# Kernel optimization log

Measured on AMD Instinct MI355X. Metric: run time of the kernel, lower is better.

The kernel has to match this reference:

```python
import jax, jax.numpy as jnp
import numpy as np

HEADS = 8
MEM_LEN = 32


def _mha(q, k, v, Wq, bq, Wk, bk, Wv, bv, Wo, bo):
    # torch nn.MultiheadAttention, batch_first=False. q: [Lq,B,E], k/v: [Lk,B,E]
    Lq, B, E = q.shape
    d = E // HEADS

    def proj(t, W, b):
        p = t @ W.T + b
        return p.reshape(t.shape[0], B, HEADS, d).transpose(1, 2, 0, 3)  # [B,h,L,d]

    qh, kh, vh = proj(q, Wq, bq), proj(k, Wk, bk), proj(v, Wv, bv)
    scale = 1.0 / jnp.sqrt(jnp.asarray(d, q.dtype))
    att = jax.nn.softmax(jnp.einsum('bhqd,bhkd->bhqk', qh * scale, kh), axis=-1)
    out = jnp.einsum('bhqk,bhkd->bhqd', att, vh)          # [B,h,Lq,d]
    out = out.transpose(2, 0, 1, 3).reshape(Lq, B, E)
    return out @ Wo.T + bo


def _forward(x, h, c, memK, memV, externalK, externalV,
             W_ih, W_hh, b_ih, b_hh,
             sWq, sbq, sWk, sbk, sWv, sbv, sWo, sbo,
             cWq, cbq, cWk, cbk, cWv, cbv, cWo, cbo,
             Wres, bres, Wrout, brout, Wcomp, bcomp, Wexp, bexp, Wgate, bgate):
    H = h.shape[1]
    # LSTMCell (torch gate order i, f, g, o)
    gates = x @ W_ih.T + b_ih + h @ W_hh.T + b_hh
    i, f, g, o = jnp.split(gates, 4, axis=1)
    c_next = jax.nn.sigmoid(f) * c + jax.nn.sigmoid(i) * jnp.tanh(g)
    h_lstm = jax.nn.sigmoid(o) * jnp.tanh(c_next)
    # append detached h_lstm to short memory, keep last MEM_LEN entries
    cur = jax.lax.stop_gradient(h_lstm)[None]                      # [1,B,H]
    memK_new = jnp.concatenate([memK, cur], axis=0)[-MEM_LEN:]     # [ML,B,H]
    memV_new = jnp.concatenate([memV, cur], axis=0)[-MEM_LEN:]
    qSelf = h_lstm[None]                                           # [1,B,H]
    self_out = _mha(qSelf, memK_new, memV_new, sWq, sbq, sWk, sbk, sWv, sbv, sWo, sbo)[0]
    ext_out = _mha(qSelf, externalK, externalV, cWq, cbq, cWk, cbk, cWv, cbv, cWo, cbo)[0]
    rw = jax.nn.softmax(h_lstm @ Wrout.T + brout, axis=1)          # [B,2] router
    routed_attn = rw[:, :1] * self_out + rw[:, 1:2] * ext_out
    routed = h_lstm + routed_attn + routed_attn @ Wres.T + bres
    temporal_summary = memK_new.mean(axis=0)                       # [B,H]
    compressed = temporal_summary @ Wcomp.T + bcomp                # [B,H//4]
    expanded = compressed @ Wexp.T + bexp                          # [B,H]
    reps = -(-H // compressed.shape[1])
    compressed_expanded = jnp.tile(compressed, (1, reps))[:, :H]
    gate = jax.nn.sigmoid(jnp.concatenate([x, routed], axis=1) @ Wgate.T + bgate)
    hCT = compressed_expanded + gate * (expanded - compressed_expanded)  # torch.lerp
    hFinal = (h_lstm + routed + hCT) / 3.0                         # dropout = identity (eval)
    return hFinal, h_lstm, c_next


def setup_inputs() -> dict:
    key = jax.random.key(0)
    ks = jax.random.split(key, 34)
    B, I, H, ML, EL = 2048, 1024, 1024, 32, 32
    BN = H // 4
    rn = lambda k, s, sc=1.0: jax.random.normal(k, s, dtype=jnp.float32) * sc
    return {
        'x': rn(ks[0], (B, I)), 'h': rn(ks[1], (B, H)), 'c': rn(ks[2], (B, H)),
        'memK': rn(ks[3], (ML, B, H)), 'memV': rn(ks[4], (ML, B, H)),
        'externalK': rn(ks[5], (EL, B, H)), 'externalV': rn(ks[6], (EL, B, H)),
        'W_ih': rn(ks[7], (4 * H, I), 0.02), 'W_hh': rn(ks[8], (4 * H, H), 0.02),
        'b_ih': jnp.zeros((4 * H,), jnp.float32), 'b_hh': jnp.zeros((4 * H,), jnp.float32),
        'sWq': rn(ks[9], (H, H), 0.02), 'sbq': rn(ks[10], (H,), 0.02),
        'sWk': rn(ks[11], (H, H), 0.02), 'sbk': rn(ks[12], (H,), 0.02),
        'sWv': rn(ks[13], (H, H), 0.02), 'sbv': rn(ks[14], (H,), 0.02),
        'sWo': rn(ks[15], (H, H), 0.02), 'sbo': rn(ks[16], (H,), 0.02),
        'cWq': rn(ks[17], (H, H), 0.02), 'cbq': rn(ks[18], (H,), 0.02),
        'cWk': rn(ks[19], (H, H), 0.02), 'cbk': rn(ks[20], (H,), 0.02),
        'cWv': rn(ks[21], (H, H), 0.02), 'cbv': rn(ks[22], (H,), 0.02),
        'cWo': rn(ks[23], (H, H), 0.02), 'cbo': rn(ks[24], (H,), 0.02),
        'Wres': rn(ks[25], (H, H), 0.02), 'bres': rn(ks[26], (H,), 0.02),
        'Wrout': rn(ks[27], (2, H), 0.02), 'brout': rn(ks[28], (2,), 0.02),
        'Wcomp': rn(ks[29], (BN, H), 0.02), 'bcomp': rn(ks[30], (BN,), 0.02),
        'Wexp': rn(ks[31], (H, BN), 0.02), 'bexp': rn(ks[32], (H,), 0.02),
        'Wgate': rn(ks[33], (H, I + H), 0.02), 'bgate': jnp.zeros((H,), jnp.float32),
    }


def reference(x, h, c, memK, memV, externalK, externalV,
              W_ih, W_hh, b_ih, b_hh,
              sWq, sbq, sWk, sbk, sWv, sbv, sWo, sbo,
              cWq, cbq, cWk, cbk, cWv, cbv, cWo, cbo,
              Wres, bres, Wrout, brout, Wcomp, bcomp, Wexp, bexp, Wgate, bgate):
    return _forward(x, h, c, memK, memV, externalK, externalV,
                    W_ih, W_hh, b_ih, b_hh,
                    sWq, sbq, sWk, sbk, sWv, sbv, sWo, sbo,
                    cWq, cbq, cWk, cbk, cWv, cbv, cWo, cbo,
                    Wres, bres, Wrout, brout, Wcomp, bcomp, Wexp, bexp, Wgate, bgate)
```

## Files before the change

### kernel.cpp

```cpp
#include <hip/hip_runtime.h>
#include <math.h>

typedef __attribute__((ext_vector_type(4))) float f32x4;
typedef __attribute__((ext_vector_type(8))) short bf16x8;
typedef __attribute__((ext_vector_type(4))) unsigned short u16x4;
typedef __attribute__((ext_vector_type(8))) unsigned short u16x8;

__device__ __forceinline__ unsigned short f2bf(float f) {
  unsigned u = __builtin_bit_cast(unsigned, f);
  u += 0x7fffu + ((u >> 16) & 1u);
  return (unsigned short)(u >> 16);
}
__device__ __forceinline__ float bf2f(unsigned short s) {
  return __builtin_bit_cast(float, (unsigned)s << 16);
}
__device__ __forceinline__ float sigmoidf_(float x) { return 1.f / (1.f + __expf(-x)); }

template <int TN, int ACAT, int BCAT, int EPI, int ABF16, int OBF16>
__global__ __launch_bounds__(256) void gemm_k(
    const void* __restrict__ A1, const void* __restrict__ A1b, int lda1, long aZ,
    const void* __restrict__ A2, int lda2, int Ksplit,
    const float* __restrict__ B1, const float* __restrict__ B1b, int ldb1, long bZ,
    const float* __restrict__ B2, int ldb2,
    const float* __restrict__ bias1, const float* __restrict__ bias1b, long biasZ,
    const float* __restrict__ bias2,
    void* __restrict__ C, void* __restrict__ Cb, int ldc, long cZ,
    int K, int zs, float scale,
    const float* __restrict__ P0, const float* __restrict__ P1,
    const float* __restrict__ P2, const float* __restrict__ P3) {
  constexpr int NBI = TN / 32;
  __shared__ unsigned short As[2][128][32];
  __shared__ unsigned short Bs[2][TN][32];
  const int t = threadIdx.x;
  const int lane = t & 63;
  const int wave = t >> 6;
  const int wr = wave >> 1, wc = wave & 1;

  const unsigned gx = gridDim.x, gy = gridDim.y;
  unsigned L = blockIdx.x + gx * (blockIdx.y + gy * blockIdx.z);
  const unsigned nwg = gx * gy * gridDim.z;
  L = (L & 7u) * (nwg >> 3) + (L >> 3);
  const int bn = L % gx;
  const unsigned r1 = L / gx;
  const int bm = r1 % gy;
  const int z = r1 / gy;

  const bool hi = z >= zs;
  const int zz = hi ? z - zs : z;
  const char* Abase = (const char*)(hi ? A1b : A1) + (long)zz * aZ * (ABF16 ? 2 : 4);
  const float* Bbase = (hi ? B1b : B1) + (long)zz * bZ;
  const float* biasp = hi ? bias1b : bias1;
  char* Czc = (char*)(hi ? Cb : C) + (long)zz * cZ * (OBF16 ? 2 : 4);

  const int ar = t >> 3;
  const int bc = (t & 7) * 4;

  const int kIters = K >> 5;
  u16x4 Ra[4], Rb[NBI];

  auto loadT = [&](int kt) {
    const int k0 = kt << 5;
    const char* Ap; int ldA, kA;
    if (ACAT == 1 && k0 >= Ksplit) { Ap = (const char*)A2; ldA = lda2; kA = k0 - Ksplit; }
    else { Ap = Abase; ldA = lda1; kA = k0; }
    const float* Bp; int ldB, kB;
    if (BCAT == 1 && k0 >= Ksplit) { Bp = B2; ldB = ldb2; kB = k0 - Ksplit; }
    else { Bp = Bbase; ldB = ldb1; kB = k0; }
#pragma unroll
    for (int i = 0; i < 4; ++i) {
      const long aoff = ((long)bm * 128 + ar + 32 * i) * ldA + kA + bc;
      if (ABF16) {
        Ra[i] = *(const u16x4*)((const unsigned short*)Ap + aoff);
      } else {
        f32x4 v = *(const f32x4*)((const float*)Ap + aoff);
        u16x4 pk;
        pk[0] = f2bf(v[0]); pk[1] = f2bf(v[1]); pk[2] = f2bf(v[2]); pk[3] = f2bf(v[3]);
        Ra[i] = pk;
      }
    }
#pragma unroll
    for (int i = 0; i < NBI; ++i) {
      f32x4 bv = *(const f32x4*)(Bp + ((long)bn * TN + ar + 32 * i) * ldB + kB + bc);
      u16x4 bp;
      bp[0] = f2bf(bv[0]); bp[1] = f2bf(bv[1]); bp[2] = f2bf(bv[2]); bp[3] = f2bf(bv[3]);
      Rb[i] = bp;
    }
  };

  loadT(0);

  f32x4 acc[4][NBI] = {};
  int p = 0;
  for (int kt = 0; kt < kIters; ++kt) {
    __syncthreads();
#pragma unroll
    for (int i = 0; i < 4; ++i) *(u16x4*)&As[p][ar + 32 * i][bc] = Ra[i];
#pragma unroll
    for (int i = 0; i < NBI; ++i) *(u16x4*)&Bs[p][ar + 32 * i][bc] = Rb[i];
    if (kt + 1 < kIters) loadT(kt + 1);
    __syncthreads();

    bf16x8 af[4], bfr[NBI];
#pragma unroll
    for (int mi = 0; mi < 4; ++mi)
      af[mi] = *(const bf16x8*)&As[p][wr * 64 + mi * 16 + (lane & 15)][(lane >> 4) * 8];
#pragma unroll
    for (int ni = 0; ni < NBI; ++ni)
      bfr[ni] = *(const bf16x8*)&Bs[p][wc * (TN / 2) + ni * 16 + (lane & 15)][(lane >> 4) * 8];
#pragma unroll
    for (int mi = 0; mi < 4; ++mi)
#pragma unroll
      for (int ni = 0; ni < NBI; ++ni)
        acc[mi][ni] = __builtin_amdgcn_mfma_f32_16x16x32_bf16(af[mi], bfr[ni], acc[mi][ni], 0, 0, 0);
    p ^= 1;
  }

  const int colb = bn * TN + wc * (TN / 2);
  const int rowb = bm * 128 + wr * 64;
#pragma unroll
  for (int mi = 0; mi < 4; ++mi) {
#pragma unroll
    for (int ni = 0; ni < NBI; ++ni) {
      f32x4 v = acc[mi][ni];
      const int col = colb + ni * 16 + (lane & 15);
      const int row0 = rowb + mi * 16 + ((lane >> 4) << 2);
      float bsum = 0.f;
      if (biasp) bsum += biasp[zz * biasZ + col];
      if (bias2) bsum += bias2[col];
#pragma unroll
      for (int q = 0; q < 4; ++q) {
        const long row = row0 + q;
        const long off = row * ldc + col;
        const float val = v[q] + bsum;
        if (EPI == 0) {
          if (OBF16) ((unsigned short*)Czc)[off] = f2bf(val * scale);
          else       ((float*)Czc)[off] = val * scale;
        } else if (EPI == 1) {
          ((float*)Czc)[off] = val + P0[off] + P1[off];
        } else if (EPI == 2) {
          const float g = sigmoidf_(val);
          const float ce = P0[row * 256 + (col & 255)];
          const float ex = P1[off];
          ((float*)Czc)[off] = (P2[off] + P3[off] + ce + g * (ex - ce)) * (1.f / 3.f);
        } else if (EPI == 3) {
          ((unsigned short*)Czc)[off] = f2bf(val * P0[2 * row + (hi ? 1 : 0)]);
        } else {
          ((float*)Czc)[off] = val + P2[2 * row] * P0[col] + P2[2 * row + 1] * P1[col];
        }
      }
    }
  }
}

__global__ __launch_bounds__(256) void transpose_k(const float* __restrict__ in0,
                                                   float* __restrict__ out0,
                                                   const float* __restrict__ in1,
                                                   float* __restrict__ out1, int n) {
  __shared__ float tile[64][65];
  const float* in = blockIdx.z ? in1 : in0;
  float* out = blockIdx.z ? out1 : out0;
  const int tr = blockIdx.y, tc = blockIdx.x, t = threadIdx.x;
#pragma unroll
  for (int it = 0; it < 16; ++it) {
    int idx = t + 256 * it;
    int r = idx >> 6, c = idx & 63;
    tile[r][c] = in[(long)(tr * 64 + r) * n + tc * 64 + c];
  }
  __syncthreads();
#pragma unroll
  for (int it = 0; it < 16; ++it) {
    int idx = t + 256 * it;
    int rr = idx >> 6, cc = idx & 63;
    out[(long)(tc * 64 + rr) * n + tr * 64 + cc] = tile[cc][rr];
  }
}

__global__ __launch_bounds__(256) void lstm_k(const float* __restrict__ gates,
                                              const float* __restrict__ c_in,
                                              const float* __restrict__ Wr,
                                              const float* __restrict__ br,
                                              float* __restrict__ c_out,
                                              float* __restrict__ h_ws,
                                              float* __restrict__ h_out,
                                              float* __restrict__ rw) {
  const int b = blockIdx.x, t = threadIdx.x;
  const long base = (long)b * 1024 + t * 4;
  const float* gb = gates + (long)b * 4096 + t * 4;
  f32x4 gi = *(const f32x4*)(gb);
  f32x4 gf = *(const f32x4*)(gb + 1024);
  f32x4 gg = *(const f32x4*)(gb + 2048);
  f32x4 go = *(const f32x4*)(gb + 3072);
  f32x4 cv = *(const f32x4*)(c_in + base);
  f32x4 cn, hv;
#pragma unroll
  for (int q = 0; q < 4; ++q) {
    float cc = sigmoidf_(gf[q]) * cv[q] + sigmoidf_(gi[q]) * tanhf(gg[q]);
    cn[q] = cc;
    hv[q] = sigmoidf_(go[q]) * tanhf(cc);
  }
  *(f32x4*)(c_out + base) = cn;
  *(f32x4*)(h_ws + base) = hv;
  *(f32x4*)(h_out + base) = hv;
  f32x4 w0 = *(const f32x4*)(Wr + t * 4);
  f32x4 w1 = *(const f32x4*)(Wr + 1024 + t * 4);
  float a0 = hv[0] * w0[0] + hv[1] * w0[1] + hv[2] * w0[2] + hv[3] * w0[3];
  float a1 = hv[0] * w1[0] + hv[1] * w1[1] + hv[2] * w1[2] + hv[3] * w1[3];
#pragma unroll
  for (int m = 32; m >= 1; m >>= 1) {
    a0 += __shfl_xor(a0, m);
    a1 += __shfl_xor(a1, m);
  }
  __shared__ float red[8];
  if ((t & 63) == 0) { red[t >> 6] = a0; red[4 + (t >> 6)] = a1; }
  __syncthreads();
  if (t == 0) {
    float z0 = red[0] + red[1] + red[2] + red[3] + br[0];
    float z1 = red[4] + red[5] + red[6] + red[7] + br[1];
    float mx = fmaxf(z0, z1);
    float e0 = __expf(z0 - mx), e1 = __expf(z1 - mx);
    float s = e0 + e1;
    rw[2 * b] = e0 / s;
    rw[2 * b + 1] = e1 / s;
  }
}

__global__ __launch_bounds__(256) void attn5_k(
    const float* __restrict__ memK, const float* __restrict__ memV,
    const float* __restrict__ extK, const float* __restrict__ extV,
    const float* __restrict__ hl,
    const unsigned short* __restrict__ qtS, const unsigned short* __restrict__ qtE,
    unsigned short* __restrict__ mixS, unsigned short* __restrict__ mixE,
    float* __restrict__ ts) {
  const int NB = 2048, H = 1024;
  __shared__ float qtf[8][1028];
  __shared__ float S_lds[32][8];
  __shared__ float P_lds[32][8];
  const int b = blockIdx.x;
  const bool self = blockIdx.y == 0;
  const int t = threadIdx.x;

  auto krow = [&](int r_) -> const float* {
    return self ? ((r_ < 31) ? memK + ((long)(r_ + 1) * NB + b) * H : hl + (long)b * H)
                : extK + ((long)r_ * NB + b) * H;
  };
  auto vrow = [&](int r_) -> const float* {
    return self ? ((r_ < 31) ? memV + ((long)(r_ + 1) * NB + b) * H : hl + (long)b * H)
                : extV + ((long)r_ * NB + b) * H;
  };

  {
    const unsigned short* qtb = (self ? qtS : qtE) + (long)b * 8192;
#pragma unroll
    for (int i = 0; i < 4; ++i) {
      const int idx = t + 256 * i;
      u16x8 qv = *(const u16x8*)(qtb + idx * 8);
      const int hh = idx >> 7, pos = (idx & 127) * 8;
      f32x4 lo, hi2;
      lo[0] = bf2f(qv[0]); lo[1] = bf2f(qv[1]); lo[2] = bf2f(qv[2]); lo[3] = bf2f(qv[3]);
      hi2[0] = bf2f(qv[4]); hi2[1] = bf2f(qv[5]); hi2[2] = bf2f(qv[6]); hi2[3] = bf2f(qv[7]);
      *(f32x4*)&qtf[hh][pos] = lo;
      *(f32x4*)&qtf[hh][pos + 4] = hi2;
    }
  }
  __syncthreads();

  const int r = t >> 3, sub = t & 7;
  const float* Kr = krow(r) + sub * 4;
  float s[8] = {};
#pragma unroll
  for (int j = 0; j < 32; j += 4) {
    f32x4 kc[4];
#pragma unroll
    for (int u = 0; u < 4; ++u) kc[u] = *(const f32x4*)(Kr + (j + u) * 32);
#pragma unroll
    for (int u = 0; u < 4; ++u) {
      const int kk = ((j + u) * 8 + sub) * 4;
#pragma unroll
      for (int hh = 0; hh < 8; ++hh) {
        f32x4 q = *(const f32x4*)&qtf[hh][kk];
        s[hh] += kc[u][0] * q[0] + kc[u][1] * q[1] + kc[u][2] * q[2] + kc[u][3] * q[3];
      }
    }
  }
#pragma unroll
  for (int hh = 0; hh < 8; ++hh) {
    s[hh] += __shfl_xor(s[hh], 1);
    s[hh] += __shfl_xor(s[hh], 2);
    s[hh] += __shfl_xor(s[hh], 4);
  }
  if (sub == 0) {
#pragma unroll
    for (int hh = 0; hh < 8; ++hh) S_lds[r][hh] = s[hh];
  }
  __syncthreads();

  {
    const int rr = t & 31, hh = t >> 5;
    float Sv = S_lds[rr][hh];
    float mx = Sv;
#pragma unroll
    for (int m = 16; m >= 1; m >>= 1) mx = fmaxf(mx, __shfl_xor(mx, m, 32));
    float pr = __expf(Sv - mx);
    float su = pr;
#pragma unroll
    for (int m = 16; m >= 1; m >>= 1) su += __shfl_xor(su, m, 32);
    P_lds[rr][hh] = pr / su;
  }
  __syncthreads();

  if (self) {
    f32x4 a = {};
#pragma unroll
    for (int l = 0; l < 32; ++l) {
      f32x4 kv = *(const f32x4*)(krow(l) + 4 * t);
      a += kv;
    }
    *(f32x4*)(ts + (long)b * H + 4 * t) = a * (1.f / 32.f);
  }

  f32x4 acc[8] = {};
#pragma unroll
  for (int l = 0; l < 32; l += 4) {
    f32x4 vv[4];
#pragma unroll
    for (int u = 0; u < 4; ++u) vv[u] = *(const f32x4*)(vrow(l + u) + 4 * t);
#pragma unroll
    for (int u = 0; u < 4; ++u) {
      f32x4 pa = *(const f32x4*)&P_lds[l + u][0];
      f32x4 pb = *(const f32x4*)&P_lds[l + u][4];
#pragma unroll
      for (int hh = 0; hh < 4; ++hh) {
        acc[hh] += pa[hh] * vv[u];
        acc[4 + hh] += pb[hh] * vv[u];
      }
    }
  }
  unsigned short* mixp = (self ? mixS : mixE) + (long)b * 8192;
#pragma unroll
  for (int hh = 0; hh < 8; ++hh) {
    u16x4 pk;
    pk[0] = f2bf(acc[hh][0]); pk[1] = f2bf(acc[hh][1]);
    pk[2] = f2bf(acc[hh][2]); pk[3] = f2bf(acc[hh][3]);
    *(u16x4*)(mixp + hh * 1024 + 4 * t) = pk;
  }
}

extern "C" void kernel_launch(void* const* d_in, const int* in_sizes, int n_in,
                              void* d_out, int out_size, void* d_ws, size_t ws_size,
                              hipStream_t stream) {
  const float* x    = (const float*)d_in[0];
  const float* h    = (const float*)d_in[1];
  const float* c    = (const float*)d_in[2];
  const float* memK = (const float*)d_in[3];
  const float* memV = (const float*)d_in[4];
  const float* extK = (const float*)d_in[5];
  const float* extV = (const float*)d_in[6];
  const float* W_ih = (const float*)d_in[7];
  const float* W_hh = (const float*)d_in[8];
  const float* b_ih = (const float*)d_in[9];
  const float* b_hh = (const float*)d_in[10];
  const float* sWq = (const float*)d_in[11];
  const float* sbq = (const float*)d_in[12];
  const float* sWk = (const float*)d_in[13];
  const float* sWv = (const float*)d_in[15];
  const float* sbv = (const float*)d_in[16];
  const float* sWo = (const float*)d_in[17];
  const float* sbo = (const float*)d_in[18];
  const float* cWq = (const float*)d_in[19];
  const float* cbq = (const float*)d_in[20];
  const float* cWk = (const float*)d_in[21];
  const float* cWv = (const float*)d_in[23];
  const float* cbv = (const float*)d_in[24];
  const float* cWo = (const float*)d_in[25];
  const float* cbo = (const float*)d_in[26];
  const float* Wres = (const float*)d_in[27];
  const float* bres = (const float*)d_in[28];
  const float* Wrout = (const float*)d_in[29];
  const float* brout = (const float*)d_in[30];
  const float* Wcomp = (const float*)d_in[31];
  const float* bcomp = (const float*)d_in[32];
  const float* Wexp = (const float*)d_in[33];
  const float* bexp = (const float*)d_in[34];
  const float* Wgate = (const float*)d_in[35];
  const float* bgate = (const float*)d_in[36];
  (void)in_sizes; (void)n_in; (void)out_size; (void)ws_size;

  float* out = (float*)d_out;
  float* w = (float*)d_ws;
  const long M1 = 1024 * 1024;
  float* gates   = w;
  float* hl      = w + 8 * M1;
  unsigned short* qsS = (unsigned short*)(w + 10 * M1);
  unsigned short* qsE = (unsigned short*)(w + 12 * M1);
  float* wkTs    = w + 14 * M1;
  float* wkTc    = w + 15 * M1;
  unsigned short* qtS = (unsigned short*)(w + 16 * M1);
  unsigned short* qtE = (unsigned short*)(w + 32 * M1);
  unsigned short* mixS = (unsigned short*)(w + 48 * M1);
  unsigned short* mixE = (unsigned short*)(w + 64 * M1);
  float* ts      = w + 80 * M1;
  unsigned short* attnS = (unsigned short*)(w + 82 * M1);
  unsigned short* attnE = (unsigned short*)(w + 84 * M1);
  float* rw      = w + 90 * M1;
  float* rattn   = w + 91 * M1;
  float* routed  = w + 93 * M1;
  float* comp    = w + 95 * M1;
  float* expd    = w + 96 * M1;

  float* hFinal_out = out;
  float* hl_out     = out + 2 * M1;
  float* cn_out     = out + 4 * M1;

  const float scaleq = 0.08838834764831845f;
  const int ZBIG = 1 << 30;
  dim3 blk(256);
  const float* nf = nullptr;

  gemm_k<128, 1, 1, 0, 0, 0><<<dim3(32, 16, 1), blk, 0, stream>>>(
      x, nullptr, 1024, 0, h, 1024, 1024,
      W_ih, nf, 1024, 0, W_hh, 1024,
      b_ih, nf, 0, b_hh,
      gates, nullptr, 4096, 0,
      2048, ZBIG, 1.f, nf, nf, nf, nf);

  transpose_k<<<dim3(16, 16, 2), blk, 0, stream>>>(sWk, wkTs, cWk, wkTc, 1024);

  lstm_k<<<2048, blk, 0, stream>>>(gates, c, Wrout, brout, cn_out, hl, hl_out, rw);

  gemm_k<128, 0, 0, 0, 0, 1><<<dim3(8, 16, 2), blk, 0, stream>>>(
      hl, hl, 1024, 0, nullptr, 0, 0,
      sWq, cWq, 1024, 0, nf, 0,
      sbq, cbq, 0, nf,
      qsS, qsE, 1024, 0,
      1024, 1, scaleq, nf, nf, nf, nf);

  gemm_k<128, 0, 0, 0, 1, 1><<<dim3(8, 16, 16), blk, 0, stream>>>(
      qsS, qsE, 1024, 128, nullptr, 0, 0,
      wkTs, wkTc, 1024, 128, nf, 0,
      nf, nf, 0, nf,
      qtS, qtE, 8192, 1024,
      128, 8, 1.f, nf, nf, nf, nf);

  attn5_k<<<dim3(2048, 2), blk, 0, stream>>>(memK, memV, extK, extV, hl,
                                             qtS, qtE, mixS, mixE, ts);

  gemm_k<64, 0, 0, 3, 1, 1><<<dim3(2, 16, 16), blk, 0, stream>>>(
      mixS, mixE, 8192, 1024, nullptr, 0, 0,
      sWv, cWv, 1024, 131072, nf, 0,
      sbv, cbv, 128, nf,
      attnS, attnE, 1024, 128,
      1024, 8, 1.f, rw, nf, nf, nf);

  gemm_k<64, 1, 1, 4, 1, 0><<<dim3(16, 16, 1), blk, 0, stream>>>(
      attnS, nullptr, 1024, 0, attnE, 1024, 1024,
      sWo, nf, 1024, 0, cWo, 1024,
      nf, nf, 0, nf,
      rattn, nullptr, 1024, 0,
      2048, ZBIG, 1.f, sbo, cbo, rw, nf);

  gemm_k<64, 0, 0, 1, 0, 0><<<dim3(16, 16, 1), blk, 0, stream>>>(
      rattn, nullptr, 1024, 0, nullptr, 0, 0,
      Wres, nf, 1024, 0, nf, 0,
      bres, nf, 0, nf,
      routed, nullptr, 1024, 0,
      1024, ZBIG, 1.f, hl, rattn, nf, nf);

  gemm_k<64, 0, 0, 0, 0, 0><<<dim3(4, 16, 1), blk, 0, stream>>>(
      ts, nullptr, 1024, 0, nullptr, 0, 0,
      Wcomp, nf, 1024, 0, nf, 0,
      bcomp, nf, 0, nf,
      comp, nullptr, 256, 0,
      1024, ZBIG, 1.f, nf, nf, nf, nf);
  gemm_k<64, 0, 0, 0, 0, 0><<<dim3(16, 16, 1), blk, 0, stream>>>(
      comp, nullptr, 256, 0, nullptr, 0, 0,
      Wexp, nf, 256, 0, nf, 0,
      bexp, nf, 0, nf,
      expd, nullptr, 1024, 0,
      256, ZBIG, 1.f, nf, nf, nf, nf);

  gemm_k<64, 1, 0, 2, 0, 0><<<dim3(16, 16, 1), blk, 0, stream>>>(
      x, nullptr, 1024, 0, routed, 1024, 1024,
      Wgate, nf, 2048, 0, nf, 0,
      bgate, nf, 0, nf,
      hFinal_out, nullptr, 1024, 0,
      2048, ZBIG, 1.f, comp, expd, hl, routed);
}
```

Baseline: 807.4 us.

## Split fused attention kernel into separate scores and mix kernels, two batches per block

The single attention kernel is replaced by two kernels. One computes scores, the softmax and the temporal mean, writing the probabilities to workspace. The other reads those probabilities and does the weighted V sum. Each 512-thread block now handles two batch rows, with 16 lanes per key row instead of 8. This aims to separate the K-phase and V-phase memory streams and to shorten per-block serial work. The cost is an extra launch and a global round trip for the probabilities. The probabilities buffer also aliases the gates workspace, which is no longer needed at that point.

```diff
diff --git a/kernel.cpp b/kernel.cpp
--- a/kernel.cpp
+++ b/kernel.cpp
@@ -224,79 +224,83 @@
   }
 }
 
-__global__ __launch_bounds__(256) void attn5_k(
-    const float* __restrict__ memK, const float* __restrict__ memV,
-    const float* __restrict__ extK, const float* __restrict__ extV,
+__global__ __launch_bounds__(512) void scores6_k(
+    const float* __restrict__ memK, const float* __restrict__ extK,
     const float* __restrict__ hl,
     const unsigned short* __restrict__ qtS, const unsigned short* __restrict__ qtE,
-    unsigned short* __restrict__ mixS, unsigned short* __restrict__ mixE,
-    float* __restrict__ ts) {
+    float* __restrict__ P_g, float* __restrict__ ts) {
   const int NB = 2048, H = 1024;
-  __shared__ float qtf[8][1028];
-  __shared__ float S_lds[32][8];
-  __shared__ float P_lds[32][8];
-  const int b = blockIdx.x;
+  __shared__ float qtf[16][1028];
+  __shared__ float S_lds[2][32][8];
+  const int b0 = blockIdx.x * 2;
   const bool self = blockIdx.y == 0;
   const int t = threadIdx.x;
 
-  auto krow = [&](int r_) -> const float* {
-    return self ? ((r_ < 31) ? memK + ((long)(r_ + 1) * NB + b) * H : hl + (long)b * H)
-                : extK + ((long)r_ * NB + b) * H;
+  auto krow = [&](int r_, int b_) -> const float* {
+    return self ? ((r_ < 31) ? memK + ((long)(r_ + 1) * NB + b_) * H : hl + (long)b_ * H)
+                : extK + ((long)r_ * NB + b_) * H;
   };
-  auto vrow = [&](int r_) -> const float* {
-    return self ? ((r_ < 31) ? memV + ((long)(r_ + 1) * NB + b) * H : hl + (long)b * H)
-                : extV + ((long)r_ * NB + b) * H;
-  };
 
   {
-    const unsigned short* qtb = (self ? qtS : qtE) + (long)b * 8192;
+    const unsigned short* qtb = (self ? qtS : qtE);
 #pragma unroll
     for (int i = 0; i < 4; ++i) {
-      const int idx = t + 256 * i;
-      u16x8 qv = *(const u16x8*)(qtb + idx * 8);
-      const int hh = idx >> 7, pos = (idx & 127) * 8;
+      const int g = t + 512 * i;
+      const int bi = g >> 10, rest = g & 1023;
+      const int hh = rest >> 7, pos = (rest & 127) * 8;
+      u16x8 qv = *(const u16x8*)(qtb + ((long)(b0 + bi) * 8192) + hh * 1024 + pos);
       f32x4 lo, hi2;
       lo[0] = bf2f(qv[0]); lo[1] = bf2f(qv[1]); lo[2] = bf2f(qv[2]); lo[3] = bf2f(qv[3]);
       hi2[0] = bf2f(qv[4]); hi2[1] = bf2f(qv[5]); hi2[2] = bf2f(qv[6]); hi2[3] = bf2f(qv[7]);
-      *(f32x4*)&qtf[hh][pos] = lo;
-      *(f32x4*)&qtf[hh][pos + 4] = hi2;
+      *(f32x4*)&qtf[bi * 8 + hh][pos] = lo;
+      *(f32x4*)&qtf[bi * 8 + hh][pos + 4] = hi2;
     }
   }
   __syncthreads();
 
-  const int r = t >> 3, sub = t & 7;
-  const float* Kr = krow(r) + sub * 4;
-  float s[8] = {};
-#pragma unroll
-  for (int j = 0; j < 32; j += 4) {
-    f32x4 kc[4];
-#pragma unroll
-    for (int u = 0; u < 4; ++u) kc[u] = *(const f32x4*)(Kr + (j + u) * 32);
+  const int r = t >> 4, sub = t & 15;
+  const float* Kr0 = krow(r, b0) + sub * 4;
+  const float* Kr1 = krow(r, b0 + 1) + sub * 4;
+  float s[2][8] = {};
+#pragma unroll
+  for (int j = 0; j < 16; j += 4) {
+    f32x4 kc0[4], kc1[4];
+#pragma unroll
+    for (int u = 0; u < 4; ++u) kc0[u] = *(const f32x4*)(Kr0 + (j + u) * 64);
+#pragma unroll
+    for (int u = 0; u < 4; ++u) kc1[u] = *(const f32x4*)(Kr1 + (j + u) * 64);
 #pragma unroll
     for (int u = 0; u < 4; ++u) {
-      const int kk = ((j + u) * 8 + sub) * 4;
+      const int kk = (j + u) * 64 + sub * 4;
 #pragma unroll
       for (int hh = 0; hh < 8; ++hh) {
-        f32x4 q = *(const f32x4*)&qtf[hh][kk];
-        s[hh] += kc[u][0] * q[0] + kc[u][1] * q[1] + kc[u][2] * q[2] + kc[u][3] * q[3];
+        f32x4 q0 = *(const f32x4*)&qtf[hh][kk];
+        f32x4 q1 = *(const f32x4*)&qtf[8 + hh][kk];
+        s[0][hh] += kc0[u][0] * q0[0] + kc0[u][1] * q0[1] + kc0[u][2] * q0[2] + kc0[u][3] * q0[3];
+        s[1][hh] += kc1[u][0] * q1[0] + kc1[u][1] * q1[1] + kc1[u][2] * q1[2] + kc1[u][3] * q1[3];
       }
     }
   }
 #pragma unroll
-  for (int hh = 0; hh < 8; ++hh) {
-    s[hh] += __shfl_xor(s[hh], 1);
-    s[hh] += __shfl_xor(s[hh], 2);
-    s[hh] += __shfl_xor(s[hh], 4);
-  }
+  for (int bi = 0; bi < 2; ++bi)
+#pragma unroll
+    for (int hh = 0; hh < 8; ++hh) {
+      s[bi][hh] += __shfl_xor(s[bi][hh], 1);
+      s[bi][hh] += __shfl_xor(s[bi][hh], 2);
+      s[bi][hh] += __shfl_xor(s[bi][hh], 4);
+      s[bi][hh] += __shfl_xor(s[bi][hh], 8);
+    }
   if (sub == 0) {
 #pragma unroll
-    for (int hh = 0; hh < 8; ++hh) S_lds[r][hh] = s[hh];
+    for (int bi = 0; bi < 2; ++bi)
+#pragma unroll
+      for (int hh = 0; hh < 8; ++hh) S_lds[bi][r][hh] = s[bi][hh];
   }
   __syncthreads();
 
   {
-    const int rr = t & 31, hh = t >> 5;
-    float Sv = S_lds[rr][hh];
+    const int bi = t >> 8, l = t & 31, hh = (t >> 5) & 7;
+    float Sv = S_lds[bi][l][hh];
     float mx = Sv;
 #pragma unroll
     for (int m = 16; m >= 1; m >>= 1) mx = fmaxf(mx, __shfl_xor(mx, m, 32));
@@ -304,35 +308,53 @@
     float su = pr;
 #pragma unroll
     for (int m = 16; m >= 1; m >>= 1) su += __shfl_xor(su, m, 32);
-    P_lds[rr][hh] = pr / su;
-  }
+    pr /= su;
+    P_g[(((long)(b0 + bi) * 2) + blockIdx.y) * 256 + l * 8 + hh] = pr;
+  }
+
+  if (self) {
+    const int bi = t >> 8, c = t & 255;
+    f32x4 a = {};
+#pragma unroll
+    for (int l = 0; l < 32; ++l) {
+      a += *(const f32x4*)(krow(l, b0 + bi) + c * 4);
+    }
+    *(f32x4*)(ts + (long)(b0 + bi) * H + c * 4) = a * (1.f / 32.f);
+  }
+}
+
+__global__ __launch_bounds__(512) void mix6_k(
+    const float* __restrict__ memV, const float* __restrict__ extV,
+    const float* __restrict__ hl,
+    const float* __restrict__ P_g,
+    unsigned short* __restrict__ mixS, unsigned short* __restrict__ mixE) {
+  const int NB = 2048, H = 1024;
+  __shared__ float P_lds[2][256];
+  const int b0 = blockIdx.x * 2;
+  const bool self = blockIdx.y == 0;
+  const int t = threadIdx.x;
+  const int bi = t >> 8, c = t & 255;
+
+  auto vrow = [&](int r_, int b_) -> const float* {
+    return self ? ((r_ < 31) ? memV + ((long)(r_ + 1) * NB + b_) * H : hl + (long)b_ * H)
+                : extV + ((long)r_ * NB + b_) * H;
+  };
+
+  P_lds[bi][c] = P_g[(((long)(b0 + bi) * 2) + blockIdx.y) * 256 + c];
   __syncthreads();
 
-  if (self) {
-    f32x4 a = {};
-#pragma unroll
-    for (int l = 0; l < 32; ++l) {
-      f32x4 kv = *(const f32x4*)(krow(l) + 4 * t);
-      a += kv;
-    }
-    *(f32x4*)(ts + (long)b * H + 4 * t) = a * (1.f / 32.f);
-  }
-
+  const int b = b0 + bi;
   f32x4 acc[8] = {};
 #pragma unroll
   for (int l = 0; l < 32; l += 4) {
     f32x4 vv[4];
 #pragma unroll
-    for (int u = 0; u < 4; ++u) vv[u] = *(const f32x4*)(vrow(l + u) + 4 * t);
+    for (int u = 0; u < 4; ++u) vv[u] = *(const f32x4*)(vrow(l + u, b) + c * 4);
 #pragma unroll
     for (int u = 0; u < 4; ++u) {
-      f32x4 pa = *(const f32x4*)&P_lds[l + u][0];
-      f32x4 pb = *(const f32x4*)&P_lds[l + u][4];
-#pragma unroll
-      for (int hh = 0; hh < 4; ++hh) {
-        acc[hh] += pa[hh] * vv[u];
-        acc[4 + hh] += pb[hh] * vv[u];
-      }
+      const float* Pl = &P_lds[bi][(l + u) * 8];
+#pragma unroll
+      for (int hh = 0; hh < 8; ++hh) acc[hh] += Pl[hh] * vv[u];
     }
   }
   unsigned short* mixp = (self ? mixS : mixE) + (long)b * 8192;
@@ -341,7 +363,7 @@
     u16x4 pk;
     pk[0] = f2bf(acc[hh][0]); pk[1] = f2bf(acc[hh][1]);
     pk[2] = f2bf(acc[hh][2]); pk[3] = f2bf(acc[hh][3]);
-    *(u16x4*)(mixp + hh * 1024 + 4 * t) = pk;
+    *(u16x4*)(mixp + hh * 1024 + c * 4) = pk;
   }
 }
 
@@ -389,6 +411,7 @@
   float* w = (float*)d_ws;
   const long M1 = 1024 * 1024;
   float* gates   = w;
+  float* P_g     = w;
   float* hl      = w + 8 * M1;
   unsigned short* qsS = (unsigned short*)(w + 10 * M1);
   unsigned short* qsE = (unsigned short*)(w + 12 * M1);
@@ -441,8 +464,8 @@
       qtS, qtE, 8192, 1024,
       128, 8, 1.f, nf, nf, nf, nf);
 
-  attn5_k<<<dim3(2048, 2), blk, 0, stream>>>(memK, memV, extK, extV, hl,
-                                             qtS, qtE, mixS, mixE, ts);
+  scores6_k<<<dim3(1024, 2), dim3(512), 0, stream>>>(memK, extK, hl, qtS, qtE, P_g, ts);
+  mix6_k<<<dim3(1024, 2), dim3(512), 0, stream>>>(memV, extV, hl, P_g, mixS, mixE);
 
   gemm_k<64, 0, 0, 3, 1, 1><<<dim3(2, 16, 16), blk, 0, stream>>>(
       mixS, mixE, 8192, 1024, nullptr, 0, 0,
```

Result: slower. 857.4 us (+6.2%).

## Split attention into separate score and mix kernels with bf16 LDS query

Applied to the files above, without the earlier changes.

The fused attention kernel becomes two kernels. The first computes scores, softmax and the temporal mean, keeps the query in LDS as bf16 in a transposed layout, and writes the probabilities to a global buffer that reuses the gates region. The second reads those probabilities and mixes V. Smaller LDS footprints and occupancy hints in launch_bounds aim to raise occupancy on these bandwidth-bound passes, and a block-index swizzle spreads consecutive blocks across the grid. The cost is an extra launch plus a small global round trip for the probabilities.

```diff
diff --git a/kernel.cpp b/kernel.cpp
--- a/kernel.cpp
+++ b/kernel.cpp
@@ -224,79 +224,69 @@
   }
 }
 
-__global__ __launch_bounds__(256) void attn5_k(
-    const float* __restrict__ memK, const float* __restrict__ memV,
-    const float* __restrict__ extK, const float* __restrict__ extV,
+__global__ __launch_bounds__(256, 6) void scores7_k(
+    const float* __restrict__ memK, const float* __restrict__ extK,
     const float* __restrict__ hl,
     const unsigned short* __restrict__ qtS, const unsigned short* __restrict__ qtE,
-    unsigned short* __restrict__ mixS, unsigned short* __restrict__ mixE,
-    float* __restrict__ ts) {
+    float* __restrict__ P_g, float* __restrict__ ts) {
   const int NB = 2048, H = 1024;
-  __shared__ float qtf[8][1028];
+  __shared__ unsigned short qt4[256 * 36];
   __shared__ float S_lds[32][8];
-  __shared__ float P_lds[32][8];
-  const int b = blockIdx.x;
-  const bool self = blockIdx.y == 0;
+  unsigned flat = blockIdx.x + gridDim.x * blockIdx.y;
+  flat = (flat & 7u) * 512u + (flat >> 3);
+  const int b = flat & 2047;
+  const bool self = (flat >> 11) == 0;
   const int t = threadIdx.x;
-
-  auto krow = [&](int r_) -> const float* {
-    return self ? ((r_ < 31) ? memK + ((long)(r_ + 1) * NB + b) * H : hl + (long)b * H)
-                : extK + ((long)r_ * NB + b) * H;
-  };
-  auto vrow = [&](int r_) -> const float* {
-    return self ? ((r_ < 31) ? memV + ((long)(r_ + 1) * NB + b) * H : hl + (long)b * H)
-                : extV + ((long)r_ * NB + b) * H;
-  };
 
   {
     const unsigned short* qtb = (self ? qtS : qtE) + (long)b * 8192;
 #pragma unroll
     for (int i = 0; i < 4; ++i) {
-      const int idx = t + 256 * i;
-      u16x8 qv = *(const u16x8*)(qtb + idx * 8);
-      const int hh = idx >> 7, pos = (idx & 127) * 8;
-      f32x4 lo, hi2;
-      lo[0] = bf2f(qv[0]); lo[1] = bf2f(qv[1]); lo[2] = bf2f(qv[2]); lo[3] = bf2f(qv[3]);
-      hi2[0] = bf2f(qv[4]); hi2[1] = bf2f(qv[5]); hi2[2] = bf2f(qv[6]); hi2[3] = bf2f(qv[7]);
-      *(f32x4*)&qtf[hh][pos] = lo;
-      *(f32x4*)&qtf[hh][pos + 4] = hi2;
+      const int chunk = t + 256 * i;
+      const int hh = chunk >> 7;
+      const int pos = (chunk & 127) * 8;
+      u16x8 qv = *(const u16x8*)(qtb + hh * 1024 + pos);
+      const int kq0 = pos >> 2;
+      *(u16x4*)&qt4[kq0 * 36 + hh * 4] = (u16x4){qv[0], qv[1], qv[2], qv[3]};
+      *(u16x4*)&qt4[(kq0 + 1) * 36 + hh * 4] = (u16x4){qv[4], qv[5], qv[6], qv[7]};
     }
   }
   __syncthreads();
 
   const int r = t >> 3, sub = t & 7;
-  const float* Kr = krow(r) + sub * 4;
-  float s[8] = {};
-#pragma unroll
-  for (int j = 0; j < 32; j += 4) {
-    f32x4 kc[4];
-#pragma unroll
-    for (int u = 0; u < 4; ++u) kc[u] = *(const f32x4*)(Kr + (j + u) * 32);
+  const float* Kr = self ? ((r < 31) ? memK + ((long)(r + 1) * NB + b) * H : hl + (long)b * H)
+                         : extK + ((long)r * NB + b) * H;
+  float acc[8] = {};
+#pragma unroll
+  for (int i = 0; i < 32; i += 4) {
+    f32x4 kv[4];
+#pragma unroll
+    for (int u = 0; u < 4; ++u) kv[u] = *(const f32x4*)(Kr + ((i + u) * 8 + sub) * 4);
 #pragma unroll
     for (int u = 0; u < 4; ++u) {
-      const int kk = ((j + u) * 8 + sub) * 4;
+      const unsigned short* qp = &qt4[((i + u) * 8 + sub) * 36];
 #pragma unroll
       for (int hh = 0; hh < 8; ++hh) {
-        f32x4 q = *(const f32x4*)&qtf[hh][kk];
-        s[hh] += kc[u][0] * q[0] + kc[u][1] * q[1] + kc[u][2] * q[2] + kc[u][3] * q[3];
+        u16x4 q = *(const u16x4*)(qp + hh * 4);
+        acc[hh] += kv[u][0] * bf2f(q[0]) + kv[u][1] * bf2f(q[1]) +
+                   kv[u][2] * bf2f(q[2]) + kv[u][3] * bf2f(q[3]);
       }
     }
   }
 #pragma unroll
   for (int hh = 0; hh < 8; ++hh) {
-    s[hh] += __shfl_xor(s[hh], 1);
-    s[hh] += __shfl_xor(s[hh], 2);
-    s[hh] += __shfl_xor(s[hh], 4);
+    acc[hh] += __shfl_xor(acc[hh], 1);
+    acc[hh] += __shfl_xor(acc[hh], 2);
+    acc[hh] += __shfl_xor(acc[hh], 4);
   }
   if (sub == 0) {
 #pragma unroll
-    for (int hh = 0; hh < 8; ++hh) S_lds[r][hh] = s[hh];
+    for (int hh = 0; hh < 8; ++hh) S_lds[r][hh] = acc[hh];
   }
   __syncthreads();
-
   {
-    const int rr = t & 31, hh = t >> 5;
-    float Sv = S_lds[rr][hh];
+    const int l = t & 31, hh = t >> 5;
+    float Sv = S_lds[l][hh];
     float mx = Sv;
 #pragma unroll
     for (int m = 16; m >= 1; m >>= 1) mx = fmaxf(mx, __shfl_xor(mx, m, 32));
@@ -304,35 +294,51 @@
     float su = pr;
 #pragma unroll
     for (int m = 16; m >= 1; m >>= 1) su += __shfl_xor(su, m, 32);
-    P_lds[rr][hh] = pr / su;
-  }
+    P_g[((long)b * 2 + (self ? 0 : 1)) * 256 + l * 8 + hh] = pr / su;
+  }
+  if (self) {
+    const float* Kb = memK + (long)b * H + 4 * t;
+    f32x4 a = {};
+#pragma unroll
+    for (int l = 0; l < 31; ++l) a += *(const f32x4*)(Kb + (long)(l + 1) * NB * H);
+    a += *(const f32x4*)(hl + (long)b * H + 4 * t);
+    *(f32x4*)(ts + (long)b * H + 4 * t) = a * (1.f / 32.f);
+  }
+}
+
+__global__ __launch_bounds__(256, 8) void mix7_k(
+    const float* __restrict__ memV, const float* __restrict__ extV,
+    const float* __restrict__ hl,
+    const float* __restrict__ P_g,
+    unsigned short* __restrict__ mixS, unsigned short* __restrict__ mixE) {
+  const int NB = 2048, H = 1024;
+  __shared__ float P_lds[256];
+  unsigned flat = blockIdx.x + gridDim.x * blockIdx.y;
+  flat = (flat & 7u) * 512u + (flat >> 3);
+  const int b = flat & 2047;
+  const bool self = (flat >> 11) == 0;
+  const int t = threadIdx.x;
+
+  P_lds[t] = P_g[((long)b * 2 + (self ? 0 : 1)) * 256 + t];
   __syncthreads();
 
-  if (self) {
-    f32x4 a = {};
-#pragma unroll
-    for (int l = 0; l < 32; ++l) {
-      f32x4 kv = *(const f32x4*)(krow(l) + 4 * t);
-      a += kv;
-    }
-    *(f32x4*)(ts + (long)b * H + 4 * t) = a * (1.f / 32.f);
-  }
-
+  const float* Vbase = (self ? memV + (long)NB * H : extV) + (long)b * H + 4 * t;
+  const float* hlp = hl + (long)b * H + 4 * t;
   f32x4 acc[8] = {};
 #pragma unroll
   for (int l = 0; l < 32; l += 4) {
     f32x4 vv[4];
 #pragma unroll
-    for (int u = 0; u < 4; ++u) vv[u] = *(const f32x4*)(vrow(l + u) + 4 * t);
-#pragma unroll
     for (int u = 0; u < 4; ++u) {
-      f32x4 pa = *(const f32x4*)&P_lds[l + u][0];
-      f32x4 pb = *(const f32x4*)&P_lds[l + u][4];
-#pragma unroll
-      for (int hh = 0; hh < 4; ++hh) {
-        acc[hh] += pa[hh] * vv[u];
-        acc[4 + hh] += pb[hh] * vv[u];
-      }
+      const int rr = l + u;
+      const float* Vr = (self && rr == 31) ? hlp : (Vbase + (long)rr * NB * H);
+      vv[u] = *(const f32x4*)Vr;
+    }
+#pragma unroll
+    for (int u = 0; u < 4; ++u) {
+      const float* Pl = &P_lds[(l + u) * 8];
+#pragma unroll
+      for (int hh = 0; hh < 8; ++hh) acc[hh] += Pl[hh] * vv[u];
     }
   }
   unsigned short* mixp = (self ? mixS : mixE) + (long)b * 8192;
@@ -389,6 +395,7 @@
   float* w = (float*)d_ws;
   const long M1 = 1024 * 1024;
   float* gates   = w;
+  float* P_g     = w;
   float* hl      = w + 8 * M1;
   unsigned short* qsS = (unsigned short*)(w + 10 * M1);
   unsigned short* qsE = (unsigned short*)(w + 12 * M1);
@@ -441,8 +448,8 @@
       qtS, qtE, 8192, 1024,
       128, 8, 1.f, nf, nf, nf, nf);
 
-  attn5_k<<<dim3(2048, 2), blk, 0, stream>>>(memK, memV, extK, extV, hl,
-                                             qtS, qtE, mixS, mixE, ts);
+  scores7_k<<<dim3(2048, 2), blk, 0, stream>>>(memK, extK, hl, qtS, qtE, P_g, ts);
+  mix7_k<<<dim3(2048, 2), blk, 0, stream>>>(memV, extV, hl, P_g, mixS, mixE);
 
   gemm_k<64, 0, 0, 3, 1, 1><<<dim3(2, 16, 16), blk, 0, stream>>>(
       mixS, mixE, 8192, 1024, nullptr, 0, 0,
```

New measurement: 1.688 ms. 109% more time.
